# Kernel tuning notes

Hardware: AMD Instinct MI355X
Metric: run time of the kernel (lower is better)

Reference implementation:

```python
import jax, jax.numpy as jnp
import numpy as np

N_NODES = 100000
N_EDGES = 1600000
IN_DIM = 128
HID = 128
OUT = 64


def gcn_conv(x, src, dst, W, b, n_nodes):
    # x: [N, Din] -> [N, Dout]; symmetric-normalized GCN with self-loops (PyG GCNConv defaults)
    h = x @ W  # transform first (as PyG does)
    loop = jnp.arange(n_nodes, dtype=src.dtype)
    s = jnp.concatenate([src, loop])
    d = jnp.concatenate([dst, loop])
    deg = jax.ops.segment_sum(jnp.ones_like(d, dtype=h.dtype), d, num_segments=n_nodes)
    dis = jnp.where(deg > 0, jax.lax.rsqrt(deg), 0.0)
    norm = dis[s] * dis[d]  # [E+N]
    msgs = h[s] * norm[:, None]  # gather-transform
    out = jax.ops.segment_sum(msgs, d, num_segments=n_nodes)  # scatter-add
    return out + b


def setup_inputs() -> dict:
    key = jax.random.key(0)
    ks = jax.random.split(key, 12)
    x = jax.random.normal(ks[0], (N_NODES, IN_DIM), dtype=jnp.float32)
    edge_index = jax.random.randint(ks[1], (2, N_EDGES), 0, N_NODES, dtype=jnp.int32)
    def lin(k, fan_in, fan_out):
        bound = 1.0 / np.sqrt(fan_in)
        kw, kb = jax.random.split(k)
        W = jax.random.uniform(kw, (fan_in, fan_out), minval=-bound, maxval=bound, dtype=jnp.float32)
        b = jax.random.uniform(kb, (fan_out,), minval=-bound, maxval=bound, dtype=jnp.float32)
        return W, b
    W1, b1 = lin(ks[2], IN_DIM, HID)
    W2, b2 = lin(ks[3], HID, HID)
    Wp1, bp1 = lin(ks[4], HID, HID)
    Wp2, bp2 = lin(ks[5], HID, OUT)
    return {"x": x, "edge_index": edge_index,
            "W1": W1, "b1": b1, "W2": W2, "b2": b2,
            "Wp1": Wp1, "bp1": bp1, "Wp2": Wp2, "bp2": bp2}


def reference(x, edge_index, W1, b1, W2, b2, Wp1, bp1, Wp2, bp2):
    n = x.shape[0]
    src, dst = edge_index[0], edge_index[1]
    # layer 1: GCNConv + relu (dropout inactive at eval)
    h = jax.nn.relu(gcn_conv(x, src, dst, W1, b1, n))
    # layer 2
    h = jax.nn.relu(gcn_conv(h, src, dst, W2, b2, n))
    # post MLP head
    h = h @ Wp1 + bp1
    h = h @ Wp2 + bp2
    return jax.nn.log_softmax(h, axis=1)
```

## Files before the change

kernel.cpp:

```cpp
#include <hip/hip_runtime.h>
#include <hip/hip_bf16.h>
#include <cstdint>

typedef __attribute__((ext_vector_type(8))) short short8;
typedef __attribute__((ext_vector_type(16))) float f32x16;
typedef unsigned short us;

#define BIN_SHIFT 9
#define BIN_NODES 512
#define CAPB 12288
#define EPB 4096

__device__ __forceinline__ float bflo(uint32_t u) { return __builtin_bit_cast(float, u << 16); }
__device__ __forceinline__ float bfhi(uint32_t u) { return __builtin_bit_cast(float, u & 0xffff0000u); }

__device__ __forceinline__ us f32_to_bf16_rne(float f) {
  uint32_t u = __builtin_bit_cast(uint32_t, f);
  u += 0x7fffu + ((u >> 16) & 1u);
  return (us)(u >> 16);
}

__device__ __forceinline__ void split2(float f, us& h, us& l) {
  uint32_t u = __builtin_bit_cast(uint32_t, f);
  h = (us)(u >> 16);
  float fh = __builtin_bit_cast(float, u & 0xffff0000u);
  float r = f - fh;
  l = (us)(__builtin_bit_cast(uint32_t, r) >> 16);
}

__global__ __launch_bounds__(256) void k_binA(
    const int* __restrict__ src, const int* __restrict__ dst,
    uint2* __restrict__ binbuf, int* __restrict__ gcur, int E, int nbins) {
  __shared__ uint2 stage[EPB];
  __shared__ int cnt[256], base[256], cur[256], gbase[256];
  int tid = threadIdx.x;
  int e0 = blockIdx.x * EPB;
  int ne = min(EPB, E - e0);
  if (ne <= 0) return;
  cnt[tid] = 0;
  __syncthreads();
  for (int i = tid; i < ne; i += 256) atomicAdd(&cnt[dst[e0 + i] >> BIN_SHIFT], 1);
  __syncthreads();
  if (tid < 64) {
    int carry = 0;
#pragma unroll
    for (int c = 0; c < 4; ++c) {
      int v = cnt[c * 64 + tid];
      int incl = v;
#pragma unroll
      for (int off = 1; off < 64; off <<= 1) {
        int t = __shfl_up(incl, off, 64);
        if (tid >= off) incl += t;
      }
      base[c * 64 + tid] = carry + incl - v;
      carry += __shfl(incl, 63, 64);
    }
  }
  __syncthreads();
  if (tid < nbins && cnt[tid] > 0) gbase[tid] = atomicAdd(&gcur[tid], cnt[tid]);
  cur[tid] = base[tid];
  __syncthreads();
  for (int i = tid; i < ne; i += 256) {
    int d = dst[e0 + i], s = src[e0 + i];
    int p = atomicAdd(&cur[d >> BIN_SHIFT], 1);
    stage[p] = make_uint2((unsigned)d, (unsigned)s);
  }
  __syncthreads();
  for (int i = tid; i < ne; i += 256) {
    uint2 en = stage[i];
    int b = en.x >> BIN_SHIFT;
    int gi = gbase[b] + (i - base[b]);
    if (gi < CAPB) binbuf[(size_t)b * CAPB + gi] = en;
  }
}

__global__ __launch_bounds__(256) void k_passB(
    const uint2* __restrict__ binbuf, const int* __restrict__ gcur,
    int* __restrict__ deg, float* __restrict__ dis, int* __restrict__ start,
    int* __restrict__ col, int N, int nbins) {
  __shared__ int hist[512], lstart[512], cur[512];
  __shared__ int colstage[CAPB];
  __shared__ int binbase_s;
  int b = blockIdx.x, tid = threadIdx.x;
  int node0 = b << BIN_SHIFT;
  int cnt = min(gcur[b], CAPB);
  hist[tid] = 0; hist[tid + 256] = 0;
  __syncthreads();
  const uint2* bp = binbuf + (size_t)b * CAPB;
  for (int i = tid; i < cnt; i += 256) atomicAdd(&hist[bp[i].x & (BIN_NODES - 1)], 1);
  __syncthreads();
  if (tid < 64) {
    int s = 0;
    for (int i = tid; i < b; i += 64) s += min(gcur[i], CAPB);
#pragma unroll
    for (int off = 32; off; off >>= 1) s += __shfl_xor(s, off, 64);
    if (tid == 0) binbase_s = s;
    int carry = 0;
#pragma unroll
    for (int c = 0; c < 8; ++c) {
      int v = hist[c * 64 + tid];
      int incl = v;
#pragma unroll
      for (int off = 1; off < 64; off <<= 1) {
        int t = __shfl_up(incl, off, 64);
        if (tid >= off) incl += t;
      }
      lstart[c * 64 + tid] = carry + incl - v;
      carry += __shfl(incl, 63, 64);
    }
  }
  __syncthreads();
  int binbase = binbase_s;
  for (int i = tid; i < 512; i += 256) {
    int node = node0 + i;
    if (node < N) {
      int dg = hist[i];
      deg[node] = dg;
      dis[node] = rsqrtf((float)(dg + 1));
      start[node] = binbase + lstart[i];
    }
  }
  cur[tid] = lstart[tid]; cur[tid + 256] = lstart[tid + 256];
  __syncthreads();
  for (int i = tid; i < cnt; i += 256) {
    uint2 en = bp[i];
    int p = atomicAdd(&cur[en.x & (BIN_NODES - 1)], 1);
    colstage[p] = (int)en.y;
  }
  __syncthreads();
  for (int i = tid; i < cnt; i += 256) col[binbase + i] = colstage[i];
}

__global__ void k_prep(const float* __restrict__ W1, const float* __restrict__ W2,
                       const float* __restrict__ Wp1, const float* __restrict__ Wp2,
                       const float* __restrict__ bp1, const float* __restrict__ bp2,
                       us* __restrict__ Wt1h, us* __restrict__ Wt1l,
                       us* __restrict__ Wt2h, us* __restrict__ Wt2l,
                       us* __restrict__ Wch, us* __restrict__ Wcl, float* __restrict__ bc) {
  int blk = blockIdx.x, tid = threadIdx.x;
  if (blk < 128) {
    const float* W = (blk < 64) ? W1 : W2;
    us* Wh = (blk < 64) ? Wt1h : Wt2h;
    us* Wl = (blk < 64) ? Wt1l : Wt2l;
    int idx = (blk & 63) * 256 + tid;
    int k = idx >> 7, n = idx & 127;
    us h, l;
    split2(W[idx], h, l);
    Wh[n * 128 + k] = h;
    Wl[n * 128 + k] = l;
  } else if (blk < 160) {
    int idx = (blk - 128) * 256 + tid;
    int k = idx >> 6, j = idx & 63;
    float acc = 0.f;
    for (int t = 0; t < 128; ++t) acc += Wp1[k * 128 + t] * Wp2[t * 64 + j];
    us h, l;
    split2(acc, h, l);
    Wch[j * 128 + k] = h;
    Wcl[j * 128 + k] = l;
  } else {
    int j = tid;
    if (j < 64) {
      float acc = bp2[j];
      for (int t = 0; t < 128; ++t) acc += bp1[t] * Wp2[t * 64 + j];
      bc[j] = acc;
    }
  }
}

template <bool AF32>
__global__ __launch_bounds__(256) void k_gemm_mfma(
    const void* __restrict__ Av, const us* __restrict__ Wh,
    const us* __restrict__ Wl, const float* __restrict__ dis,
    us* __restrict__ out_bf16, int N, int ntiles) {
  __shared__ us As_hi[32 * 136];
  __shared__ us As_lo[32 * 136];
  int tid = threadIdx.x;
  int wave = tid >> 6, lane = tid & 63;
  int n0 = wave * 32;
  int nn = n0 + (lane & 31);
  int khalf = (lane >> 5) * 8;
  int m = lane & 31;

  short8 bh[8], bl[8];
#pragma unroll
  for (int c = 0; c < 8; ++c) {
    bh[c] = *(const short8*)&Wh[nn * 128 + c * 16 + khalf];
    bl[c] = *(const short8*)&Wl[nn * 128 + c * 16 + khalf];
  }

  for (int t = blockIdx.x; t < ntiles; t += gridDim.x) {
    int row0 = t * 32;
    __syncthreads();
    if (AF32) {
      const float* A = (const float*)Av;
      for (int j = tid; j < 1024; j += 256) {
        int r = j >> 5, c = j & 31;
        int row = row0 + r;
        float4 v = make_float4(0.f, 0.f, 0.f, 0.f);
        if (row < N) v = *(const float4*)&A[(size_t)row * 128 + c * 4];
        us h0, h1, h2, h3, l0, l1, l2, l3;
        split2(v.x, h0, l0); split2(v.y, h1, l1);
        split2(v.z, h2, l2); split2(v.w, h3, l3);
        *(ushort4*)&As_hi[r * 136 + c * 4] = make_ushort4(h0, h1, h2, h3);
        *(ushort4*)&As_lo[r * 136 + c * 4] = make_ushort4(l0, l1, l2, l3);
      }
    } else {
      const us* A = (const us*)Av;
      for (int j = tid; j < 512; j += 256) {
        int r = j >> 4, c = j & 15;
        int row = row0 + r;
        uint4 v = make_uint4(0u, 0u, 0u, 0u);
        if (row < N) v = *(const uint4*)&A[(size_t)row * 128 + c * 8];
        *(uint4*)&As_hi[r * 136 + c * 8] = v;
      }
    }
    __syncthreads();

    f32x16 acc = {};
#pragma unroll
    for (int c = 0; c < 8; ++c) {
      short8 ah = *(const short8*)&As_hi[m * 136 + c * 16 + khalf];
      acc = __builtin_amdgcn_mfma_f32_32x32x16_bf16(ah, bh[c], acc, 0, 0, 0);
      acc = __builtin_amdgcn_mfma_f32_32x32x16_bf16(ah, bl[c], acc, 0, 0, 0);
      if (AF32) {
        short8 al = *(const short8*)&As_lo[m * 136 + c * 16 + khalf];
        acc = __builtin_amdgcn_mfma_f32_32x32x16_bf16(al, bh[c], acc, 0, 0, 0);
      }
    }

    int col = n0 + (lane & 31);
    int rbase = row0 + 4 * (lane >> 5);
#pragma unroll
    for (int reg = 0; reg < 16; ++reg) {
      int row = rbase + (reg & 3) + 8 * (reg >> 2);
      if (row < N) {
        float v = acc[reg] * dis[row];
        out_bf16[(size_t)row * 128 + col] = f32_to_bf16_rne(v);
      }
    }
  }
}

__global__ __launch_bounds__(256) void k_gather(
    const us* __restrict__ h, us* __restrict__ o,
    const int* __restrict__ start, const int* __restrict__ deg,
    const int* __restrict__ col, const float* __restrict__ dis,
    const float* __restrict__ bias, int N) {
  int wave = threadIdx.x >> 6, lane = threadIdx.x & 63;
  int node = blockIdx.x * 4 + wave;
  if (node >= N) return;
  const uint32_t* h1 = (const uint32_t*)h;
  uint32_t u = h1[(size_t)node * 64 + lane];
  float a0 = bflo(u), b0 = bfhi(u);
  float a1 = 0.f, b1 = 0.f, a2 = 0.f, b2 = 0.f, a3 = 0.f, b3 = 0.f;
  int e0 = start[node];
  int dg = deg[node];
  int myc = (lane < dg) ? col[e0 + lane] : N;
  int dgm = min(dg, 64);
  for (int k = 0; k < dgm; k += 4) {
    int c0 = __builtin_amdgcn_readlane(myc, k);
    int c1 = __builtin_amdgcn_readlane(myc, k + 1);
    int c2 = __builtin_amdgcn_readlane(myc, k + 2);
    int c3 = __builtin_amdgcn_readlane(myc, k + 3);
    uint32_t u0 = h1[(size_t)c0 * 64 + lane];
    uint32_t u1 = h1[(size_t)c1 * 64 + lane];
    uint32_t u2 = h1[(size_t)c2 * 64 + lane];
    uint32_t u3 = h1[(size_t)c3 * 64 + lane];
    a0 += bflo(u0); b0 += bfhi(u0);
    a1 += bflo(u1); b1 += bfhi(u1);
    a2 += bflo(u2); b2 += bfhi(u2);
    a3 += bflo(u3); b3 += bfhi(u3);
  }
  for (int e = e0 + 64; e < e0 + dg; ++e) {
    uint32_t u0 = h1[(size_t)col[e] * 64 + lane];
    a0 += bflo(u0); b0 += bfhi(u0);
  }
  float sc = dis[node];
  float2 bb = ((const float2*)bias)[lane];
  float rx = fmaxf((a0 + a1 + a2 + a3) * sc + bb.x, 0.f);
  float ry = fmaxf((b0 + b1 + b2 + b3) * sc + bb.y, 0.f);
  ((uint32_t*)o)[(size_t)node * 64 + lane] =
      ((uint32_t)f32_to_bf16_rne(ry) << 16) | f32_to_bf16_rne(rx);
}

__global__ __launch_bounds__(256) void k_head_mfma(
    const us* __restrict__ act, const us* __restrict__ Wch,
    const us* __restrict__ Wcl, const float* __restrict__ bc,
    float* __restrict__ out, int N) {
  __shared__ us As[64 * 136];
  __shared__ float red[2][2][64];
  int tid = threadIdx.x;
  int wave = tid >> 6, lane = tid & 63;
  int rt = wave >> 1, ct = wave & 1;
  int colj = ct * 32 + (lane & 31);
  int khalf = (lane >> 5) * 8;
  int m = lane & 31;

  short8 bh[8], bl[8];
#pragma unroll
  for (int c = 0; c < 8; ++c) {
    bh[c] = *(const short8*)&Wch[colj * 128 + c * 16 + khalf];
    bl[c] = *(const short8*)&Wcl[colj * 128 + c * 16 + khalf];
  }

  int row0 = blockIdx.x * 64;
  for (int j = tid; j < 1024; j += 256) {
    int r = j >> 4, c = j & 15;
    int row = row0 + r;
    uint4 v = make_uint4(0u, 0u, 0u, 0u);
    if (row < N) v = *(const uint4*)&act[(size_t)row * 128 + c * 8];
    *(uint4*)&As[r * 136 + c * 8] = v;
  }
  __syncthreads();

  f32x16 acc = {};
  int mrow = rt * 32 + m;
#pragma unroll
  for (int c = 0; c < 8; ++c) {
    short8 ah = *(const short8*)&As[mrow * 136 + c * 16 + khalf];
    acc = __builtin_amdgcn_mfma_f32_32x32x16_bf16(ah, bh[c], acc, 0, 0, 0);
    acc = __builtin_amdgcn_mfma_f32_32x32x16_bf16(ah, bl[c], acc, 0, 0, 0);
  }

  float bcv = bc[colj];
  float lg[16], mx[16];
#pragma unroll
  for (int reg = 0; reg < 16; ++reg) {
    lg[reg] = acc[reg] + bcv;
    float v = lg[reg];
#pragma unroll
    for (int off = 16; off > 0; off >>= 1) v = fmaxf(v, __shfl_xor(v, off, 32));
    mx[reg] = v;
  }
  if ((lane & 31) == 0) {
#pragma unroll
    for (int reg = 0; reg < 16; ++reg) {
      int rl = rt * 32 + (reg & 3) + 8 * (reg >> 2) + 4 * (lane >> 5);
      red[0][ct][rl] = mx[reg];
    }
  }
  __syncthreads();

  float ex[16], sm[16];
#pragma unroll
  for (int reg = 0; reg < 16; ++reg) {
    int rl = rt * 32 + (reg & 3) + 8 * (reg >> 2) + 4 * (lane >> 5);
    float rmax = fmaxf(red[0][0][rl], red[0][1][rl]);
    ex[reg] = lg[reg] - rmax;
    float v = expf(ex[reg]);
#pragma unroll
    for (int off = 16; off > 0; off >>= 1) v += __shfl_xor(v, off, 32);
    sm[reg] = v;
  }
  if ((lane & 31) == 0) {
#pragma unroll
    for (int reg = 0; reg < 16; ++reg) {
      int rl = rt * 32 + (reg & 3) + 8 * (reg >> 2) + 4 * (lane >> 5);
      red[1][ct][rl] = sm[reg];
    }
  }
  __syncthreads();

#pragma unroll
  for (int reg = 0; reg < 16; ++reg) {
    int rl = rt * 32 + (reg & 3) + 8 * (reg >> 2) + 4 * (lane >> 5);
    int row = row0 + rl;
    if (row < N) {
      float total = red[1][0][rl] + red[1][1][rl];
      out[(size_t)row * 64 + colj] = ex[reg] - logf(total);
    }
  }
}

extern "C" void kernel_launch(void* const* d_in, const int* in_sizes, int n_in,
                              void* d_out, int out_size, void* d_ws, size_t ws_size,
                              hipStream_t stream) {
  const float* x   = (const float*)d_in[0];
  const int*   ei  = (const int*)d_in[1];
  const float* W1  = (const float*)d_in[2];
  const float* b1  = (const float*)d_in[3];
  const float* W2  = (const float*)d_in[4];
  const float* b2  = (const float*)d_in[5];
  const float* Wp1 = (const float*)d_in[6];
  const float* bp1 = (const float*)d_in[7];
  const float* Wp2 = (const float*)d_in[8];
  const float* bp2 = (const float*)d_in[9];
  float* out = (float*)d_out;

  int N = in_sizes[0] / 128;
  int E = in_sizes[1] / 2;
  const int* src = ei;
  const int* dst = ei + E;
  int nbins = (N + BIN_NODES - 1) >> BIN_SHIFT;

  float* dis   = (float*)d_ws;
  int*   deg   = (int*)(dis + N);
  int*   start = deg + N;
  int*   col   = start + N;
  int*   gcur  = col + ((E + 3) & ~3);
  us* Wt1h = (us*)(gcur + 256);
  us* Wt1l = Wt1h + 16384;
  us* Wt2h = Wt1l + 16384;
  us* Wt2l = Wt2h + 16384;
  us* Wch  = Wt2l + 16384;
  us* Wcl  = Wch + 8192;
  float* bc = (float*)(Wcl + 8192);
  uint2* binbuf = (uint2*)(bc + 80);
  us* hbuf = (us*)(binbuf + (size_t)nbins * CAPB);
  us* act  = hbuf + (size_t)(N + 1) * 128;

  hipMemsetAsync(gcur, 0, 256 * sizeof(int), stream);
  hipMemsetAsync(hbuf + (size_t)N * 128, 0, 128 * sizeof(us), stream);

  int ablocks = (E + EPB - 1) / EPB;
  k_binA<<<ablocks, 256, 0, stream>>>(src, dst, binbuf, gcur, E, nbins);
  k_passB<<<nbins, 256, 0, stream>>>(binbuf, gcur, deg, dis, start, col, N, nbins);
  k_prep<<<161, 256, 0, stream>>>(W1, W2, Wp1, Wp2, bp1, bp2,
                                  Wt1h, Wt1l, Wt2h, Wt2l, Wch, Wcl, bc);

  int ntiles = (N + 31) / 32;
  int gemm_grid = ntiles < 1024 ? ntiles : 1024;
  int agblocks = (N + 3) / 4;
  int hblocks = (N + 63) / 64;

  k_gemm_mfma<true><<<gemm_grid, 256, 0, stream>>>(x, Wt1h, Wt1l, dis, hbuf, N, ntiles);
  k_gather<<<agblocks, 256, 0, stream>>>(hbuf, act, start, deg, col, dis, b1, N);
  k_gemm_mfma<false><<<gemm_grid, 256, 0, stream>>>(act, Wt2h, Wt2l, dis, hbuf, N, ntiles);
  k_gather<<<agblocks, 256, 0, stream>>>(hbuf, act, start, deg, col, dis, b2, N);
  k_head_mfma<<<hblocks, 256, 0, stream>>>(act, Wch, Wcl, bc, out, N);
}
```

Measured before the change: 402.5 us.

## Drop A low-part split in layer-1 GEMM, widen gather unroll, fold memsets into prep

```diff
diff --git a/kernel.cpp b/kernel.cpp
--- a/kernel.cpp
+++ b/kernel.cpp
@@ -28,115 +28,13 @@
   l = (us)(__builtin_bit_cast(uint32_t, r) >> 16);
 }
 
-__global__ __launch_bounds__(256) void k_binA(
-    const int* __restrict__ src, const int* __restrict__ dst,
-    uint2* __restrict__ binbuf, int* __restrict__ gcur, int E, int nbins) {
-  __shared__ uint2 stage[EPB];
-  __shared__ int cnt[256], base[256], cur[256], gbase[256];
-  int tid = threadIdx.x;
-  int e0 = blockIdx.x * EPB;
-  int ne = min(EPB, E - e0);
-  if (ne <= 0) return;
-  cnt[tid] = 0;
-  __syncthreads();
-  for (int i = tid; i < ne; i += 256) atomicAdd(&cnt[dst[e0 + i] >> BIN_SHIFT], 1);
-  __syncthreads();
-  if (tid < 64) {
-    int carry = 0;
-#pragma unroll
-    for (int c = 0; c < 4; ++c) {
-      int v = cnt[c * 64 + tid];
-      int incl = v;
-#pragma unroll
-      for (int off = 1; off < 64; off <<= 1) {
-        int t = __shfl_up(incl, off, 64);
-        if (tid >= off) incl += t;
-      }
-      base[c * 64 + tid] = carry + incl - v;
-      carry += __shfl(incl, 63, 64);
-    }
-  }
-  __syncthreads();
-  if (tid < nbins && cnt[tid] > 0) gbase[tid] = atomicAdd(&gcur[tid], cnt[tid]);
-  cur[tid] = base[tid];
-  __syncthreads();
-  for (int i = tid; i < ne; i += 256) {
-    int d = dst[e0 + i], s = src[e0 + i];
-    int p = atomicAdd(&cur[d >> BIN_SHIFT], 1);
-    stage[p] = make_uint2((unsigned)d, (unsigned)s);
-  }
-  __syncthreads();
-  for (int i = tid; i < ne; i += 256) {
-    uint2 en = stage[i];
-    int b = en.x >> BIN_SHIFT;
-    int gi = gbase[b] + (i - base[b]);
-    if (gi < CAPB) binbuf[(size_t)b * CAPB + gi] = en;
-  }
-}
-
-__global__ __launch_bounds__(256) void k_passB(
-    const uint2* __restrict__ binbuf, const int* __restrict__ gcur,
-    int* __restrict__ deg, float* __restrict__ dis, int* __restrict__ start,
-    int* __restrict__ col, int N, int nbins) {
-  __shared__ int hist[512], lstart[512], cur[512];
-  __shared__ int colstage[CAPB];
-  __shared__ int binbase_s;
-  int b = blockIdx.x, tid = threadIdx.x;
-  int node0 = b << BIN_SHIFT;
-  int cnt = min(gcur[b], CAPB);
-  hist[tid] = 0; hist[tid + 256] = 0;
-  __syncthreads();
-  const uint2* bp = binbuf + (size_t)b * CAPB;
-  for (int i = tid; i < cnt; i += 256) atomicAdd(&hist[bp[i].x & (BIN_NODES - 1)], 1);
-  __syncthreads();
-  if (tid < 64) {
-    int s = 0;
-    for (int i = tid; i < b; i += 64) s += min(gcur[i], CAPB);
-#pragma unroll
-    for (int off = 32; off; off >>= 1) s += __shfl_xor(s, off, 64);
-    if (tid == 0) binbase_s = s;
-    int carry = 0;
-#pragma unroll
-    for (int c = 0; c < 8; ++c) {
-      int v = hist[c * 64 + tid];
-      int incl = v;
-#pragma unroll
-      for (int off = 1; off < 64; off <<= 1) {
-        int t = __shfl_up(incl, off, 64);
-        if (tid >= off) incl += t;
-      }
-      lstart[c * 64 + tid] = carry + incl - v;
-      carry += __shfl(incl, 63, 64);
-    }
-  }
-  __syncthreads();
-  int binbase = binbase_s;
-  for (int i = tid; i < 512; i += 256) {
-    int node = node0 + i;
-    if (node < N) {
-      int dg = hist[i];
-      deg[node] = dg;
-      dis[node] = rsqrtf((float)(dg + 1));
-      start[node] = binbase + lstart[i];
-    }
-  }
-  cur[tid] = lstart[tid]; cur[tid + 256] = lstart[tid + 256];
-  __syncthreads();
-  for (int i = tid; i < cnt; i += 256) {
-    uint2 en = bp[i];
-    int p = atomicAdd(&cur[en.x & (BIN_NODES - 1)], 1);
-    colstage[p] = (int)en.y;
-  }
-  __syncthreads();
-  for (int i = tid; i < cnt; i += 256) col[binbase + i] = colstage[i];
-}
-
 __global__ void k_prep(const float* __restrict__ W1, const float* __restrict__ W2,
                        const float* __restrict__ Wp1, const float* __restrict__ Wp2,
                        const float* __restrict__ bp1, const float* __restrict__ bp2,
                        us* __restrict__ Wt1h, us* __restrict__ Wt1l,
                        us* __restrict__ Wt2h, us* __restrict__ Wt2l,
-                       us* __restrict__ Wch, us* __restrict__ Wcl, float* __restrict__ bc) {
+                       us* __restrict__ Wch, us* __restrict__ Wcl, float* __restrict__ bc,
+                       int* __restrict__ gcur, int* __restrict__ hzero) {
   int blk = blockIdx.x, tid = threadIdx.x;
   if (blk < 128) {
     const float* W = (blk < 64) ? W1 : W2;
@@ -158,22 +56,124 @@
     Wch[j * 128 + k] = h;
     Wcl[j * 128 + k] = l;
   } else {
-    int j = tid;
-    if (j < 64) {
-      float acc = bp2[j];
-      for (int t = 0; t < 128; ++t) acc += bp1[t] * Wp2[t * 64 + j];
-      bc[j] = acc;
-    }
-  }
-}
-
-template <bool AF32>
-__global__ __launch_bounds__(256) void k_gemm_mfma(
-    const void* __restrict__ Av, const us* __restrict__ Wh,
+    gcur[tid] = 0;
+    if (tid < 64) {
+      hzero[tid] = 0;
+      float acc = bp2[tid];
+      for (int t = 0; t < 128; ++t) acc += bp1[t] * Wp2[t * 64 + tid];
+      bc[tid] = acc;
+    }
+  }
+}
+
+__global__ __launch_bounds__(256) void k_binA(
+    const int* __restrict__ src, const int* __restrict__ dst,
+    uint2* __restrict__ binbuf, int* __restrict__ gcur, int E, int nbins) {
+  __shared__ uint2 stage[EPB];
+  __shared__ int cnt[256], base[256], cur[256], gbase[256];
+  int tid = threadIdx.x;
+  int e0 = blockIdx.x * EPB;
+  int ne = min(EPB, E - e0);
+  if (ne <= 0) return;
+  cnt[tid] = 0;
+  __syncthreads();
+  for (int i = tid; i < ne; i += 256) atomicAdd(&cnt[dst[e0 + i] >> BIN_SHIFT], 1);
+  __syncthreads();
+  if (tid < 64) {
+    int carry = 0;
+#pragma unroll
+    for (int c = 0; c < 4; ++c) {
+      int v = cnt[c * 64 + tid];
+      int incl = v;
+#pragma unroll
+      for (int off = 1; off < 64; off <<= 1) {
+        int t = __shfl_up(incl, off, 64);
+        if (tid >= off) incl += t;
+      }
+      base[c * 64 + tid] = carry + incl - v;
+      carry += __shfl(incl, 63, 64);
+    }
+  }
+  __syncthreads();
+  if (tid < nbins && cnt[tid] > 0) gbase[tid] = atomicAdd(&gcur[tid], cnt[tid]);
+  cur[tid] = base[tid];
+  __syncthreads();
+  for (int i = tid; i < ne; i += 256) {
+    int d = dst[e0 + i], s = src[e0 + i];
+    int p = atomicAdd(&cur[d >> BIN_SHIFT], 1);
+    stage[p] = make_uint2((unsigned)d, (unsigned)s);
+  }
+  __syncthreads();
+  for (int i = tid; i < ne; i += 256) {
+    uint2 en = stage[i];
+    int b = en.x >> BIN_SHIFT;
+    int gi = gbase[b] + (i - base[b]);
+    if (gi < CAPB) binbuf[(size_t)b * CAPB + gi] = en;
+  }
+}
+
+__global__ __launch_bounds__(256) void k_passB(
+    const uint2* __restrict__ binbuf, const int* __restrict__ gcur,
+    int* __restrict__ deg, float* __restrict__ dis, int* __restrict__ start,
+    int* __restrict__ col, int N, int nbins) {
+  __shared__ int hist[512], lstart[512], cur[512];
+  __shared__ int colstage[CAPB];
+  __shared__ int binbase_s;
+  int b = blockIdx.x, tid = threadIdx.x;
+  int node0 = b << BIN_SHIFT;
+  int cnt = min(gcur[b], CAPB);
+  hist[tid] = 0; hist[tid + 256] = 0;
+  __syncthreads();
+  const uint2* bp = binbuf + (size_t)b * CAPB;
+  for (int i = tid; i < cnt; i += 256) atomicAdd(&hist[bp[i].x & (BIN_NODES - 1)], 1);
+  __syncthreads();
+  if (tid < 64) {
+    int s = 0;
+    for (int i = tid; i < b; i += 64) s += min(gcur[i], CAPB);
+#pragma unroll
+    for (int off = 32; off; off >>= 1) s += __shfl_xor(s, off, 64);
+    if (tid == 0) binbase_s = s;
+    int carry = 0;
+#pragma unroll
+    for (int c = 0; c < 8; ++c) {
+      int v = hist[c * 64 + tid];
+      int incl = v;
+#pragma unroll
+      for (int off = 1; off < 64; off <<= 1) {
+        int t = __shfl_up(incl, off, 64);
+        if (tid >= off) incl += t;
+      }
+      lstart[c * 64 + tid] = carry + incl - v;
+      carry += __shfl(incl, 63, 64);
+    }
+  }
+  __syncthreads();
+  int binbase = binbase_s;
+  for (int i = tid; i < 512; i += 256) {
+    int node = node0 + i;
+    if (node < N) {
+      int dg = hist[i];
+      deg[node] = dg;
+      dis[node] = rsqrtf((float)(dg + 1));
+      start[node] = binbase + lstart[i];
+    }
+  }
+  cur[tid] = lstart[tid]; cur[tid + 256] = lstart[tid + 256];
+  __syncthreads();
+  for (int i = tid; i < cnt; i += 256) {
+    uint2 en = bp[i];
+    int p = atomicAdd(&cur[en.x & (BIN_NODES - 1)], 1);
+    colstage[p] = (int)en.y;
+  }
+  __syncthreads();
+  for (int i = tid; i < cnt; i += 256) col[binbase + i] = colstage[i];
+}
+
+__global__ __launch_bounds__(256) void k_gemm1(
+    const float* __restrict__ A, const us* __restrict__ Wh,
     const us* __restrict__ Wl, const float* __restrict__ dis,
     us* __restrict__ out_bf16, int N, int ntiles) {
-  __shared__ us As_hi[32 * 136];
-  __shared__ us As_lo[32 * 136];
+  __shared__ us As[32 * 136];
   int tid = threadIdx.x;
   int wave = tid >> 6, lane = tid & 63;
   int n0 = wave * 32;
@@ -191,41 +191,23 @@
   for (int t = blockIdx.x; t < ntiles; t += gridDim.x) {
     int row0 = t * 32;
     __syncthreads();
-    if (AF32) {
-      const float* A = (const float*)Av;
-      for (int j = tid; j < 1024; j += 256) {
-        int r = j >> 5, c = j & 31;
-        int row = row0 + r;
-        float4 v = make_float4(0.f, 0.f, 0.f, 0.f);
-        if (row < N) v = *(const float4*)&A[(size_t)row * 128 + c * 4];
-        us h0, h1, h2, h3, l0, l1, l2, l3;
-        split2(v.x, h0, l0); split2(v.y, h1, l1);
-        split2(v.z, h2, l2); split2(v.w, h3, l3);
-        *(ushort4*)&As_hi[r * 136 + c * 4] = make_ushort4(h0, h1, h2, h3);
-        *(ushort4*)&As_lo[r * 136 + c * 4] = make_ushort4(l0, l1, l2, l3);
-      }
-    } else {
-      const us* A = (const us*)Av;
-      for (int j = tid; j < 512; j += 256) {
-        int r = j >> 4, c = j & 15;
-        int row = row0 + r;
-        uint4 v = make_uint4(0u, 0u, 0u, 0u);
-        if (row < N) v = *(const uint4*)&A[(size_t)row * 128 + c * 8];
-        *(uint4*)&As_hi[r * 136 + c * 8] = v;
-      }
+    for (int j = tid; j < 1024; j += 256) {
+      int r = j >> 5, c = j & 31;
+      int row = row0 + r;
+      float4 v = make_float4(0.f, 0.f, 0.f, 0.f);
+      if (row < N) v = *(const float4*)&A[(size_t)row * 128 + c * 4];
+      *(ushort4*)&As[r * 136 + c * 4] = make_ushort4(
+          f32_to_bf16_rne(v.x), f32_to_bf16_rne(v.y),
+          f32_to_bf16_rne(v.z), f32_to_bf16_rne(v.w));
     }
     __syncthreads();
 
     f32x16 acc = {};
 #pragma unroll
     for (int c = 0; c < 8; ++c) {
-      short8 ah = *(const short8*)&As_hi[m * 136 + c * 16 + khalf];
+      short8 ah = *(const short8*)&As[m * 136 + c * 16 + khalf];
       acc = __builtin_amdgcn_mfma_f32_32x32x16_bf16(ah, bh[c], acc, 0, 0, 0);
       acc = __builtin_amdgcn_mfma_f32_32x32x16_bf16(ah, bl[c], acc, 0, 0, 0);
-      if (AF32) {
-        short8 al = *(const short8*)&As_lo[m * 136 + c * 16 + khalf];
-        acc = __builtin_amdgcn_mfma_f32_32x32x16_bf16(al, bh[c], acc, 0, 0, 0);
-      }
     }
 
     int col = n0 + (lane & 31);
@@ -241,35 +223,100 @@
   }
 }
 
-__global__ __launch_bounds__(256) void k_gather(
+__global__ __launch_bounds__(256) void k_gemm2(
+    const us* __restrict__ A, const us* __restrict__ Wh,
+    const us* __restrict__ Wl, const float* __restrict__ dis,
+    us* __restrict__ out_bf16, int N, int ntiles) {
+  __shared__ us As[32 * 136];
+  int tid = threadIdx.x;
+  int wave = tid >> 6, lane = tid & 63;
+  int n0 = wave * 32;
+  int nn = n0 + (lane & 31);
+  int khalf = (lane >> 5) * 8;
+  int m = lane & 31;
+
+  short8 bh[8], bl[8];
+#pragma unroll
+  for (int c = 0; c < 8; ++c) {
+    bh[c] = *(const short8*)&Wh[nn * 128 + c * 16 + khalf];
+    bl[c] = *(const short8*)&Wl[nn * 128 + c * 16 + khalf];
+  }
+
+  for (int t = blockIdx.x; t < ntiles; t += gridDim.x) {
+    int row0 = t * 32;
+    __syncthreads();
+    for (int j = tid; j < 512; j += 256) {
+      int r = j >> 4, c = j & 15;
+      int row = row0 + r;
+      uint4 v = make_uint4(0u, 0u, 0u, 0u);
+      if (row < N) v = *(const uint4*)&A[(size_t)row * 128 + c * 8];
+      *(uint4*)&As[r * 136 + c * 8] = v;
+    }
+    __syncthreads();
+
+    f32x16 acc = {};
+#pragma unroll
+    for (int c = 0; c < 8; ++c) {
+      short8 ah = *(const short8*)&As[m * 136 + c * 16 + khalf];
+      acc = __builtin_amdgcn_mfma_f32_32x32x16_bf16(ah, bh[c], acc, 0, 0, 0);
+      acc = __builtin_amdgcn_mfma_f32_32x32x16_bf16(ah, bl[c], acc, 0, 0, 0);
+    }
+
+    int col = n0 + (lane & 31);
+    int rbase = row0 + 4 * (lane >> 5);
+#pragma unroll
+    for (int reg = 0; reg < 16; ++reg) {
+      int row = rbase + (reg & 3) + 8 * (reg >> 2);
+      if (row < N) {
+        float v = acc[reg] * dis[row];
+        out_bf16[(size_t)row * 128 + col] = f32_to_bf16_rne(v);
+      }
+    }
+  }
+}
+
+__global__ __launch_bounds__(512) void k_gather(
     const us* __restrict__ h, us* __restrict__ o,
     const int* __restrict__ start, const int* __restrict__ deg,
     const int* __restrict__ col, const float* __restrict__ dis,
     const float* __restrict__ bias, int N) {
   int wave = threadIdx.x >> 6, lane = threadIdx.x & 63;
-  int node = blockIdx.x * 4 + wave;
+  int node = blockIdx.x * 8 + wave;
   if (node >= N) return;
   const uint32_t* h1 = (const uint32_t*)h;
   uint32_t u = h1[(size_t)node * 64 + lane];
   float a0 = bflo(u), b0 = bfhi(u);
   float a1 = 0.f, b1 = 0.f, a2 = 0.f, b2 = 0.f, a3 = 0.f, b3 = 0.f;
+  float a4 = 0.f, b4 = 0.f, a5 = 0.f, b5 = 0.f, a6 = 0.f, b6 = 0.f, a7 = 0.f, b7 = 0.f;
   int e0 = start[node];
   int dg = deg[node];
   int myc = (lane < dg) ? col[e0 + lane] : N;
   int dgm = min(dg, 64);
-  for (int k = 0; k < dgm; k += 4) {
+  for (int k = 0; k < dgm; k += 8) {
     int c0 = __builtin_amdgcn_readlane(myc, k);
     int c1 = __builtin_amdgcn_readlane(myc, k + 1);
     int c2 = __builtin_amdgcn_readlane(myc, k + 2);
     int c3 = __builtin_amdgcn_readlane(myc, k + 3);
+    int c4 = __builtin_amdgcn_readlane(myc, k + 4);
+    int c5 = __builtin_amdgcn_readlane(myc, k + 5);
+    int c6 = __builtin_amdgcn_readlane(myc, k + 6);
+    int c7 = __builtin_amdgcn_readlane(myc, k + 7);
     uint32_t u0 = h1[(size_t)c0 * 64 + lane];
     uint32_t u1 = h1[(size_t)c1 * 64 + lane];
     uint32_t u2 = h1[(size_t)c2 * 64 + lane];
     uint32_t u3 = h1[(size_t)c3 * 64 + lane];
+    uint32_t u4 = h1[(size_t)c4 * 64 + lane];
+    uint32_t u5 = h1[(size_t)c5 * 64 + lane];
+    uint32_t u6 = h1[(size_t)c6 * 64 + lane];
+    uint32_t u7 = h1[(size_t)c7 * 64 + lane];
     a0 += bflo(u0); b0 += bfhi(u0);
     a1 += bflo(u1); b1 += bfhi(u1);
     a2 += bflo(u2); b2 += bfhi(u2);
     a3 += bflo(u3); b3 += bfhi(u3);
+    a4 += bflo(u4); b4 += bfhi(u4);
+    a5 += bflo(u5); b5 += bfhi(u5);
+    a6 += bflo(u6); b6 += bfhi(u6);
+    a7 += bflo(u7); b7 += bfhi(u7);
   }
   for (int e = e0 + 64; e < e0 + dg; ++e) {
     uint32_t u0 = h1[(size_t)col[e] * 64 + lane];
@@ -277,8 +324,10 @@
   }
   float sc = dis[node];
   float2 bb = ((const float2*)bias)[lane];
-  float rx = fmaxf((a0 + a1 + a2 + a3) * sc + bb.x, 0.f);
-  float ry = fmaxf((b0 + b1 + b2 + b3) * sc + bb.y, 0.f);
+  float ax = ((a0 + a1) + (a2 + a3)) + ((a4 + a5) + (a6 + a7));
+  float ay = ((b0 + b1) + (b2 + b3)) + ((b4 + b5) + (b6 + b7));
+  float rx = fmaxf(ax * sc + bb.x, 0.f);
+  float ry = fmaxf(ay * sc + bb.y, 0.f);
   ((uint32_t*)o)[(size_t)node * 64 + lane] =
       ((uint32_t)f32_to_bf16_rne(ry) << 16) | f32_to_bf16_rne(rx);
 }
@@ -409,23 +458,22 @@
   us* hbuf = (us*)(binbuf + (size_t)nbins * CAPB);
   us* act  = hbuf + (size_t)(N + 1) * 128;
 
-  hipMemsetAsync(gcur, 0, 256 * sizeof(int), stream);
-  hipMemsetAsync(hbuf + (size_t)N * 128, 0, 128 * sizeof(us), stream);
+  k_prep<<<161, 256, 0, stream>>>(W1, W2, Wp1, Wp2, bp1, bp2,
+                                  Wt1h, Wt1l, Wt2h, Wt2l, Wch, Wcl, bc,
+                                  gcur, (int*)(hbuf + (size_t)N * 128));
 
   int ablocks = (E + EPB - 1) / EPB;
   k_binA<<<ablocks, 256, 0, stream>>>(src, dst, binbuf, gcur, E, nbins);
   k_passB<<<nbins, 256, 0, stream>>>(binbuf, gcur, deg, dis, start, col, N, nbins);
-  k_prep<<<161, 256, 0, stream>>>(W1, W2, Wp1, Wp2, bp1, bp2,
-                                  Wt1h, Wt1l, Wt2h, Wt2l, Wch, Wcl, bc);
 
   int ntiles = (N + 31) / 32;
   int gemm_grid = ntiles < 1024 ? ntiles : 1024;
-  int agblocks = (N + 3) / 4;
+  int agblocks = (N + 7) / 8;
   int hblocks = (N + 63) / 64;
 
-  k_gemm_mfma<true><<<gemm_grid, 256, 0, stream>>>(x, Wt1h, Wt1l, dis, hbuf, N, ntiles);
-  k_gather<<<agblocks, 256, 0, stream>>>(hbuf, act, start, deg, col, dis, b1, N);
-  k_gemm_mfma<false><<<gemm_grid, 256, 0, stream>>>(act, Wt2h, Wt2l, dis, hbuf, N, ntiles);
-  k_gather<<<agblocks, 256, 0, stream>>>(hbuf, act, start, deg, col, dis, b2, N);
+  k_gemm1<<<gemm_grid, 256, 0, stream>>>(x, Wt1h, Wt1l, dis, hbuf, N, ntiles);
+  k_gather<<<agblocks, 512, 0, stream>>>(hbuf, act, start, deg, col, dis, b1, N);
+  k_gemm2<<<gemm_grid, 256, 0, stream>>>(act, Wt2h, Wt2l, dis, hbuf, N, ntiles);
+  k_gather<<<agblocks, 512, 0, stream>>>(hbuf, act, start, deg, col, dis, b2, N);
   k_head_mfma<<<hblocks, 256, 0, stream>>>(act, Wch, Wcl, bc, out, N);
 }
```

Result: no change. 397.8 us (-1.2%).
